# Kernel tuning notes

Measured on AMD Instinct MI355X. Metric: run time of the kernel, lower is better.

The kernel has to match this reference:

```python
import jax, jax.numpy as jnp
import numpy as np

K = 8
B = 3.0
DIM = 32
HID = 32
BATCH = 65536
MIN_BW = 1e-3
MIN_BH = 1e-3
MIN_D = 1e-3


def setup_inputs() -> dict:
    key = jax.random.key(0)
    ks = jax.random.split(key, 8)
    L = DIM - 1
    x = jax.random.normal(ks[0], (BATCH, DIM), jnp.float32)
    init_param = jax.random.uniform(ks[1], (3 * K - 1,), jnp.float32, -0.5, 0.5)
    # stacked per-dim FCNN weights; layer l conditions on x[:, :l+1] -> causal zero-mask
    w1 = jax.random.normal(ks[2], (L, L, HID), jnp.float32) * 0.2
    mask = (jnp.arange(L)[None, :] <= jnp.arange(L)[:, None]).astype(jnp.float32)
    w1 = w1 * mask[:, :, None]
    b1 = jax.random.normal(ks[3], (L, HID), jnp.float32) * 0.1
    w2 = jax.random.normal(ks[4], (L, HID, HID), jnp.float32) * 0.2
    b2 = jax.random.normal(ks[5], (L, HID), jnp.float32) * 0.1
    w3 = jax.random.normal(ks[6], (L, HID, 3 * K - 1), jnp.float32) * 0.2
    b3 = jax.random.normal(ks[7], (L, 3 * K - 1), jnp.float32) * 0.1
    return {"x": x, "init_param": init_param, "w1": w1, "b1": b1,
            "w2": w2, "b2": b2, "w3": w3, "b3": b3}


def _rqs_forward(x, Wu, Hu, Du):
    # x: [dim, batch]; Wu, Hu: [dim, batch, K]; Du: [dim, batch, K-1]
    inside = (x >= -B) & (x <= B)
    xc = jnp.clip(x, -B, B)
    # bin widths
    widths = jax.nn.softmax(Wu, axis=-1)
    widths = MIN_BW + (1.0 - MIN_BW * K) * widths
    cw = jnp.cumsum(widths, axis=-1)
    cw = jnp.concatenate([jnp.zeros(cw.shape[:-1] + (1,), cw.dtype), cw], axis=-1)
    cw = 2.0 * B * cw - B
    cw = cw.at[..., 0].set(-B).at[..., -1].set(B)
    widths = cw[..., 1:] - cw[..., :-1]
    # bin heights
    heights = jax.nn.softmax(Hu, axis=-1)
    heights = MIN_BH + (1.0 - MIN_BH * K) * heights
    ch = jnp.cumsum(heights, axis=-1)
    ch = jnp.concatenate([jnp.zeros(ch.shape[:-1] + (1,), ch.dtype), ch], axis=-1)
    ch = 2.0 * B * ch - B
    ch = ch.at[..., 0].set(-B).at[..., -1].set(B)
    heights = ch[..., 1:] - ch[..., :-1]
    # knot derivatives, edges pinned so softplus(const)+min_d = 1
    const = float(np.log(np.exp(1.0 - MIN_D) - 1.0))
    pad = jnp.full(Du.shape[:-1] + (1,), const, Du.dtype)
    derivs = MIN_D + jax.nn.softplus(jnp.concatenate([pad, Du, pad], axis=-1))  # [.., K+1]
    # bin search (searchsorted on cumwidths, eps bump on last edge)
    cw_s = cw.at[..., -1].add(1e-6)
    idx = jnp.sum((xc[..., None] >= cw_s).astype(jnp.int32), axis=-1) - 1
    idx = jnp.clip(idx, 0, K - 1)
    g = lambda a: jnp.take_along_axis(a, idx[..., None], axis=-1)[..., 0]
    in_cw = g(cw)
    in_w = g(widths)
    in_ch = g(ch)
    in_h = g(heights)
    in_delta = g(heights / widths)
    d0 = g(derivs)
    d1 = g(derivs[..., 1:])
    theta = (xc - in_cw) / in_w
    tt = theta * (1.0 - theta)
    num = in_h * (in_delta * theta ** 2 + d0 * tt)
    den = in_delta + (d0 + d1 - 2.0 * in_delta) * tt
    out = in_ch + num / den
    dnum = in_delta ** 2 * (d1 * theta ** 2 + 2.0 * in_delta * tt + d0 * (1.0 - theta) ** 2)
    ld = jnp.log(dnum) - 2.0 * jnp.log(den)
    out = jnp.where(inside, out, x)  # identity tails
    ld = jnp.where(inside, ld, 0.0)
    return out, ld


def reference(x, init_param, w1, b1, w2, b2, w3, b3):
    # all per-dim conditioners at once (w1 is causally masked in setup)
    h1 = jnp.tanh(jnp.einsum('bd,ldh->lbh', x[:, :DIM - 1], w1) + b1[:, None, :])
    h2 = jnp.tanh(jnp.einsum('lbh,lhg->lbg', h1, w2) + b2[:, None, :])
    out = jnp.einsum('lbh,lho->lbo', h2, w3) + b3[:, None, :]  # [dim-1, batch, 3K-1]
    p0 = jnp.broadcast_to(init_param, (1, x.shape[0], 3 * K - 1))
    params = jnp.concatenate([p0, out], axis=0)  # [dim, batch, 3K-1]
    Wu = 2.0 * B * jax.nn.softmax(params[..., :K], axis=-1)
    Hu = 2.0 * B * jax.nn.softmax(params[..., K:2 * K], axis=-1)
    Du = jax.nn.softplus(params[..., 2 * K:])
    z_t, ld = _rqs_forward(x.T, Wu, Hu, Du)  # [dim, batch]
    return z_t.T, jnp.sum(ld, axis=0)
```

## Files before the change

### kernel.cpp

```cpp
#include <hip/hip_runtime.h>
#include <hip/hip_bf16.h>
#include <cmath>

constexpr int KN   = 8;
constexpr int NPAR = 23;
constexpr int DD   = 32;
constexpr float BND   = 3.0f;
constexpr float MINBW = 1e-3f;
constexpr float MIND  = 1e-3f;

#define TPB   64
#define ROWS  64
#define GDIMS 4
#define WST   40
#define PSTF  28
#define RECB  8192

typedef __attribute__((ext_vector_type(8))) short short8;
typedef __attribute__((ext_vector_type(4))) float float4v;

#define RCP(x) __builtin_amdgcn_rcpf(x)

#if __has_builtin(__builtin_amdgcn_exp2f)
#define EXP2(x) __builtin_amdgcn_exp2f(x)
#else
#define EXP2(x) __expf((x) * 0.6931471805599453f)
#endif
#if __has_builtin(__builtin_amdgcn_logf)
#define LOG2F(x) __builtin_amdgcn_logf(x)
#else
#define LOG2F(x) __log2f(x)
#endif
#define MED3(x, lo, hi) __builtin_amdgcn_fmed3f((x), (lo), (hi))

constexpr float L2E = 1.4426950408889634f;
constexpr float LN2 = 0.6931471805599453f;

__device__ __forceinline__ short f2bf(float f) {
    unsigned u = __float_as_uint(f);
    u += 0x7fffu + ((u >> 16) & 1u);
    return (short)(u >> 16);
}

__device__ __forceinline__ int pkbf(float a, float b) {
    union { __hip_bfloat162 v; int i; } u;
    u.v = __float22bfloat162_rn(make_float2(a, b));
    return u.i;
}

__device__ __forceinline__ float4v tanh4v(float4v c) {
    constexpr float C2L = 2.0f * L2E;
    float4v o;
#pragma unroll
    for (int i = 0; i < 4; ++i) {
        float e = EXP2(c[i] * C2L);
        o[i] = fmaf(-2.f, RCP(e + 1.f), 1.f);
    }
    return o;
}

__device__ __forceinline__ float rqs_apply(float xv, const float* p, float& ldout) {
    constexpr float C1 = 2.0f * BND * MINBW;
    constexpr float FC = 2.0f * BND * (1.0f - MINBW * KN);

    float t0w[KN], t0h[KN];
#pragma unroll
    for (int k = 0; k < KN; ++k) t0w[k] = EXP2(p[k]);
#pragma unroll
    for (int k = 0; k < KN; ++k) t0h[k] = EXP2(p[KN + k]);
    float sw = ((t0w[0] + t0w[1]) + (t0w[2] + t0w[3]))
             + ((t0w[4] + t0w[5]) + (t0w[6] + t0w[7]));
    float sh = ((t0h[0] + t0h[1]) + (t0h[2] + t0h[3]))
             + ((t0h[4] + t0h[5]) + (t0h[6] + t0h[7]));
    float r1   = RCP(sw * sh);
    float invw = (2.0f * BND * L2E) * (r1 * sh);
    float invh = (2.0f * BND * L2E) * (r1 * sw);
    float e2w[KN], e2h[KN];
#pragma unroll
    for (int k = 0; k < KN; ++k) e2w[k] = EXP2(t0w[k] * invw);
#pragma unroll
    for (int k = 0; k < KN; ++k) e2h[k] = EXP2(t0h[k] * invh);
    float s2w = ((e2w[0] + e2w[1]) + (e2w[2] + e2w[3]))
              + ((e2w[4] + e2w[5]) + (e2w[6] + e2w[7]));
    float s2h = ((e2h[0] + e2h[1]) + (e2h[2] + e2h[3]))
              + ((e2h[4] + e2h[5]) + (e2h[6] + e2h[7]));
    float r2   = RCP(s2w * s2h);
    float facw = FC * (r2 * s2h);
    float fach = FC * (r2 * s2w);

    float xc = MED3(xv, -BND, BND);

    float w0 = fmaf(facw, e2w[0], C1);
    float h0 = fmaf(fach, e2h[0], C1);
    float in_cw = -BND, in_w = w0, in_ch = -BND, in_h = h0;
    float dl0 = 0.0f, dl1 = p[2 * KN];
    bool e0 = true, e1 = false;
    float cwk = -BND + w0;
    float chk = -BND + h0;
#pragma unroll
    for (int k = 1; k < KN; ++k) {
        float wk = fmaf(facw, e2w[k], C1);
        float hk = fmaf(fach, e2h[k], C1);
        bool c = (xc >= cwk);
        in_cw = c ? cwk : in_cw;
        in_w  = c ? wk  : in_w;
        in_ch = c ? chk : in_ch;
        in_h  = c ? hk  : in_h;
        dl0   = c ? p[2 * KN + k - 1] : dl0;
        if (k < KN - 1) dl1 = c ? p[2 * KN + k] : dl1;
        if (k == 1)      e0 = !c;
        if (k == KN - 1) e1 = c;
        cwk += wk;
        chk += hk;
    }
    in_w = e1 ? (BND - in_cw) : in_w;
    in_h = e1 ? (BND - in_ch) : in_h;

    float sp0 = LOG2F(2.0f + EXP2(dl0));
    float sp1 = LOG2F(2.0f + EXP2(dl1));
    float d0 = e0 ? 1.0f : fmaf(LN2, sp0, MIND);
    float d1 = e1 ? 1.0f : fmaf(LN2, sp1, MIND);

    float u  = xc - in_cw;
    float v  = in_w - u;
    float s  = in_w, h = in_h;
    float uu = u * u, vv = v * v, uv = u * v;
    float uvs = uv * s;
    float t   = fmaf(v, v, uu);
    float dd  = d0 + d1;
    float DEN = fmaf(h, t, dd * uvs);
    float rD  = RCP(DEN);
    float NUM = fmaf(h, uu, d0 * uvs);
    float z   = fmaf(h * NUM, rD, in_ch);
    float t2  = fmaf(d0, vv, d1 * uu);
    float DN  = fmaf(h + h, uv, t2 * s);
    float h2s = (h * h) * s;
    float larg = ((h2s * DN) * rD) * rD;

    bool inside = (xv >= -BND) && (xv <= BND);
    ldout = inside ? LN2 * LOG2F(larg) : 0.0f;
    return inside ? z : xv;
}

__device__ __forceinline__ short8 xpose_h(float4v cA, float4v cB,
                                          int sl_a, int sl_b, bool qlow) {
    float4v tA = tanh4v(cA);
    float4v tB = tanh4v(cB);
    int a0 = pkbf(tA[0], tA[1]);
    int a1 = pkbf(tA[2], tA[3]);
    int b0 = pkbf(tB[0], tB[1]);
    int b1 = pkbf(tB[2], tB[3]);
    int gA0 = __shfl(a0, sl_a, 64);
    int gA1 = __shfl(a1, sl_a, 64);
    int gA2 = __shfl(a0, sl_b, 64);
    int gA3 = __shfl(a1, sl_b, 64);
    int gB0 = __shfl(b0, sl_a, 64);
    int gB1 = __shfl(b1, sl_a, 64);
    int gB2 = __shfl(b0, sl_b, 64);
    int gB3 = __shfl(b1, sl_b, 64);
    union { int4 i; short8 s; } u;
    u.i = qlow ? make_int4(gA0, gA1, gA2, gA3) : make_int4(gB0, gB1, gB2, gB3);
    return u.s;
}

__device__ __forceinline__ float4v f4v(float4 v) {
    float4v r; r[0] = v.x; r[1] = v.y; r[2] = v.z; r[3] = v.w; return r;
}

struct WFrag {
    short8 w1a, w1b, w2a, w2b, w3a, w3b;
    float4v bA1, bB1, bA2, bB2, bA3, bB3;
};

__device__ __forceinline__ WFrag load_wfrag(const char* __restrict__ wbuf,
                                            int l, int ln, int q) {
    const char* rec = wbuf + (size_t)l * RECB;
    const short* rw = (const short*)rec;
    const float* rb = (const float*)(rec + 7680);
    WFrag f;
    f.w1a = *(const short8*)&rw[ln * WST + q * 8];
    f.w1b = *(const short8*)&rw[(16 + ln) * WST + q * 8];
    f.w2a = *(const short8*)&rw[1280 + ln * WST + q * 8];
    f.w2b = *(const short8*)&rw[1280 + (16 + ln) * WST + q * 8];
    f.w3a = *(const short8*)&rw[2560 + ln * WST + q * 8];
    f.w3b = *(const short8*)&rw[2560 + (16 + ln) * WST + q * 8];
    f.bA1 = f4v(*(const float4*)&rb[4 * q]);
    f.bB1 = f4v(*(const float4*)&rb[16 + 4 * q]);
    f.bA2 = f4v(*(const float4*)&rb[32 + 4 * q]);
    f.bB2 = f4v(*(const float4*)&rb[48 + 4 * q]);
    f.bA3 = f4v(*(const float4*)&rb[64 + 4 * q]);
    f.bB3 = f4v(*(const float4*)&rb[80 + 4 * q]);
    return f;
}

extern "C" __global__ void __launch_bounds__(256)
k_prep(const float* __restrict__ w1, const float* __restrict__ b1,
       const float* __restrict__ w2, const float* __restrict__ b2,
       const float* __restrict__ w3, const float* __restrict__ b3,
       char* __restrict__ wbuf, float* __restrict__ ldo, int B)
{
    const int l = blockIdx.x, tid = threadIdx.x;
    if (l >= 31) {
        const int zb = l - 31;
        const int chunk = B >> 6;
        float4* dst = (float4*)(ldo + (size_t)zb * chunk);
        for (int i = tid; i < (chunk >> 2); i += 256)
            dst[i] = make_float4(0.f, 0.f, 0.f, 0.f);
        return;
    }
    short* r1 = (short*)(wbuf + (size_t)l * RECB);
    short* r2 = r1 + 1280;
    short* r3 = r2 + 1280;
    float* f1 = (float*)(wbuf + (size_t)l * RECB + 7680);
    float* f2 = f1 + 32;
    float* f3 = f2 + 32;
    const float* g1 = w1 + (size_t)l * 992;
    const float* g2 = w2 + (size_t)l * 1024;
    const float* g3 = w3 + (size_t)l * 736;
    for (int i = tid; i < 1280; i += 256) {
        int n = i / WST, k = i - WST * n;
        r1[i] = (k < 31) ? f2bf(g1[k * 32 + n]) : (short)0;
        r2[i] = (k < 32) ? f2bf(g2[k * 32 + n]) : (short)0;
        r3[i] = (n < 23 && k < 32) ? f2bf(g3[k * 23 + n] * L2E) : (short)0;
    }
    if (tid < 32) { f1[tid] = b1[(size_t)l * 32 + tid]; f2[tid] = b2[(size_t)l * 32 + tid]; }
    if (tid < 32) f3[tid] = (tid < 23) ? b3[(size_t)l * 23 + tid] * L2E : 0.0f;
}

extern "C" __global__ void __launch_bounds__(TPB, 2)
k_nsf(const float* __restrict__ x,
      const float* __restrict__ p0,
      const char* __restrict__ wbuf,
      float* __restrict__ zo, float* __restrict__ ldo, int B)
{
    __shared__ __align__(16) float sPf[ROWS * PSTF];

    const int tid  = threadIdx.x;
    const int lane = tid & 63;
    const int q    = lane >> 4;
    const int ln   = lane & 15;
    const int qb   = q & 1;
    const bool qlow = (q < 2);
    const int sl_a = ln + 32 * qb;
    const int sl_b = sl_a + 16;
    const int g    = blockIdx.y;
    const int ly0  = GDIMS * g;
    const long long rowbase = (long long)blockIdx.x * ROWS;
    const long long row = rowbase + tid;

    float xarr[GDIMS];
    {
        float4 xs = *(const float4*)(x + row * DD + ly0);
        xarr[0] = xs.x; xarr[1] = xs.y; xarr[2] = xs.z; xarr[3] = xs.w;
    }

    short8 au[4];
#pragma unroll
    for (int t = 0; t < 4; ++t) {
        const int m0 = 16 * t;
        const float4* xp = (const float4*)(x + (rowbase + m0 + ln) * DD + q * 8);
        float4 uu = xp[0], vv = xp[1];
        union { int4 i; short8 s; } c;
        c.i = make_int4(pkbf(uu.x, uu.y), pkbf(uu.z, uu.w),
                        pkbf(vv.x, vv.y), pkbf(vv.z, vv.w));
        au[t] = c.s;
    }

    float zreg[GDIMS];
    float ldacc = 0.0f;

    WFrag wf = load_wfrag(wbuf, (ly0 == 0) ? 0 : ly0 - 1, ln, q);

#pragma unroll
    for (int j = 0; j < GDIMS; ++j) {
        const int ly = ly0 + j;
        if (ly == 0) {
            float pr[NPAR];
#pragma unroll
            for (int k = 0; k < NPAR; ++k) pr[k] = p0[k] * L2E;
            float ld;
            zreg[0] = rqs_apply(xarr[0], pr, ld);
            ldacc += ld;
            continue;
        }

        float4v cA[4], cB[4];
#pragma unroll
        for (int t = 0; t < 4; ++t) {
            cA[t] = __builtin_amdgcn_mfma_f32_16x16x32_bf16(wf.w1a, au[t], wf.bA1, 0, 0, 0);
            cB[t] = __builtin_amdgcn_mfma_f32_16x16x32_bf16(wf.w1b, au[t], wf.bB1, 0, 0, 0);
        }
        short8 h1f[4];
#pragma unroll
        for (int t = 0; t < 4; ++t)
            h1f[t] = xpose_h(cA[t], cB[t], sl_a, sl_b, qlow);
#pragma unroll
        for (int t = 0; t < 4; ++t) {
            cA[t] = __builtin_amdgcn_mfma_f32_16x16x32_bf16(wf.w2a, h1f[t], wf.bA2, 0, 0, 0);
            cB[t] = __builtin_amdgcn_mfma_f32_16x16x32_bf16(wf.w2b, h1f[t], wf.bB2, 0, 0, 0);
        }
#pragma unroll
        for (int t = 0; t < 4; ++t)
            h1f[t] = xpose_h(cA[t], cB[t], sl_a, sl_b, qlow);
#pragma unroll
        for (int t = 0; t < 4; ++t) {
            cA[t] = __builtin_amdgcn_mfma_f32_16x16x32_bf16(wf.w3a, h1f[t], wf.bA3, 0, 0, 0);
            cB[t] = __builtin_amdgcn_mfma_f32_16x16x32_bf16(wf.w3b, h1f[t], wf.bB3, 0, 0, 0);
        }
#pragma unroll
        for (int t = 0; t < 4; ++t) {
            const int m0 = 16 * t;
            *(float4v*)&sPf[(m0 + ln) * PSTF + 4 * q] = cA[t];
            if (qlow)
                *(float4v*)&sPf[(m0 + ln) * PSTF + 16 + 4 * q] = cB[t];
        }

        WFrag wfn;
        if (j + 1 < GDIMS) wfn = load_wfrag(wbuf, ly, ln, q);

        {
            const float* pp = &sPf[tid * PSTF];
            float pr[24];
#pragma unroll
            for (int u = 0; u < 6; ++u) {
                float4v hv = *(const float4v*)(pp + 4 * u);
                pr[4*u+0] = hv[0];
                pr[4*u+1] = hv[1];
                pr[4*u+2] = hv[2];
                pr[4*u+3] = hv[3];
            }
            float ld;
            zreg[j] = rqs_apply(xarr[j], pr, ld);
            ldacc += ld;
        }
        if (j + 1 < GDIMS) wf = wfn;
    }

    float4 zv = make_float4(zreg[0], zreg[1], zreg[2], zreg[3]);
    *(float4*)(zo + row * DD + ly0) = zv;
    unsafeAtomicAdd(&ldo[row], ldacc);
}

extern "C" void kernel_launch(void* const* d_in, const int* in_sizes, int n_in,
                              void* d_out, int out_size, void* d_ws, size_t ws_size,
                              hipStream_t stream) {
    const float* x  = (const float*)d_in[0];
    const float* p0 = (const float*)d_in[1];
    const float* w1 = (const float*)d_in[2];
    const float* b1 = (const float*)d_in[3];
    const float* w2 = (const float*)d_in[4];
    const float* b2 = (const float*)d_in[5];
    const float* w3 = (const float*)d_in[6];
    const float* b3 = (const float*)d_in[7];

    const int B = in_sizes[0] / DD;
    float* zo  = (float*)d_out;
    float* ldo = zo + (size_t)B * DD;
    char* wbuf = (char*)d_ws;

    hipLaunchKernelGGL(k_prep, dim3(95), dim3(256), 0, stream,
                       w1, b1, w2, b2, w3, b3, wbuf, ldo, B);
    hipLaunchKernelGGL(k_nsf, dim3(B / ROWS, DD / GDIMS), dim3(TPB), 0, stream,
                       x, p0, wbuf, zo, ldo, B);
}
```

Measured before the change: 132.3 us.

## Software-pipeline spline evaluation behind next dim's MFMAs and fold tanh scale

Restructures the per-dimension loop so the rational-quadratic spline for the previous dimension is evaluated after issuing the MFMA conditioner for the current dimension, double-buffering the parameter registers. This aims to overlap matrix-core latency with VALU transcendental work. It also folds the 2*log2(e) tanh scale into the packed w1/w2/b1/b2 weights, removing a multiply per activation. The change raises register pressure and alters bf16 rounding of scaled weights slightly.

```diff
diff --git a/kernel.cpp b/kernel.cpp
--- a/kernel.cpp
+++ b/kernel.cpp
@@ -34,6 +34,7 @@
 #define MED3(x, lo, hi) __builtin_amdgcn_fmed3f((x), (lo), (hi))
 
 constexpr float L2E = 1.4426950408889634f;
+constexpr float C2L = 2.0f * L2E;
 constexpr float LN2 = 0.6931471805599453f;
 
 __device__ __forceinline__ short f2bf(float f) {
@@ -49,11 +50,10 @@
 }
 
 __device__ __forceinline__ float4v tanh4v(float4v c) {
-    constexpr float C2L = 2.0f * L2E;
     float4v o;
 #pragma unroll
     for (int i = 0; i < 4; ++i) {
-        float e = EXP2(c[i] * C2L);
+        float e = EXP2(c[i]);
         o[i] = fmaf(-2.f, RCP(e + 1.f), 1.f);
     }
     return o;
@@ -219,11 +219,11 @@
     const float* g3 = w3 + (size_t)l * 736;
     for (int i = tid; i < 1280; i += 256) {
         int n = i / WST, k = i - WST * n;
-        r1[i] = (k < 31) ? f2bf(g1[k * 32 + n]) : (short)0;
-        r2[i] = (k < 32) ? f2bf(g2[k * 32 + n]) : (short)0;
+        r1[i] = (k < 31) ? f2bf(g1[k * 32 + n] * C2L) : (short)0;
+        r2[i] = (k < 32) ? f2bf(g2[k * 32 + n] * C2L) : (short)0;
         r3[i] = (n < 23 && k < 32) ? f2bf(g3[k * 23 + n] * L2E) : (short)0;
     }
-    if (tid < 32) { f1[tid] = b1[(size_t)l * 32 + tid]; f2[tid] = b2[(size_t)l * 32 + tid]; }
+    if (tid < 32) { f1[tid] = b1[(size_t)l * 32 + tid] * C2L; f2[tid] = b2[(size_t)l * 32 + tid] * C2L; }
     if (tid < 32) f3[tid] = (tid < 23) ? b3[(size_t)l * 23 + tid] * L2E : 0.0f;
 }
 
@@ -268,72 +268,76 @@
 
     float zreg[GDIMS];
     float ldacc = 0.0f;
+    float pr[2][24];
 
     WFrag wf = load_wfrag(wbuf, (ly0 == 0) ? 0 : ly0 - 1, ln, q);
 
 #pragma unroll
     for (int j = 0; j < GDIMS; ++j) {
-        const int ly = ly0 + j;
+        const int ly  = ly0 + j;
+        const int cur = j & 1;
+        WFrag wfn;
         if (ly == 0) {
-            float pr[NPAR];
-#pragma unroll
-            for (int k = 0; k < NPAR; ++k) pr[k] = p0[k] * L2E;
+#pragma unroll
+            for (int k = 0; k < NPAR; ++k) pr[0][k] = p0[k] * L2E;
+        } else {
+            float4v cA[4], cB[4];
+#pragma unroll
+            for (int t = 0; t < 4; ++t) {
+                cA[t] = __builtin_amdgcn_mfma_f32_16x16x32_bf16(wf.w1a, au[t], wf.bA1, 0, 0, 0);
+                cB[t] = __builtin_amdgcn_mfma_f32_16x16x32_bf16(wf.w1b, au[t], wf.bB1, 0, 0, 0);
+            }
+            short8 h1f[4];
+#pragma unroll
+            for (int t = 0; t < 4; ++t)
+                h1f[t] = xpose_h(cA[t], cB[t], sl_a, sl_b, qlow);
+#pragma unroll
+            for (int t = 0; t < 4; ++t) {
+                cA[t] = __builtin_amdgcn_mfma_f32_16x16x32_bf16(wf.w2a, h1f[t], wf.bA2, 0, 0, 0);
+                cB[t] = __builtin_amdgcn_mfma_f32_16x16x32_bf16(wf.w2b, h1f[t], wf.bB2, 0, 0, 0);
+            }
+#pragma unroll
+            for (int t = 0; t < 4; ++t)
+                h1f[t] = xpose_h(cA[t], cB[t], sl_a, sl_b, qlow);
+#pragma unroll
+            for (int t = 0; t < 4; ++t) {
+                cA[t] = __builtin_amdgcn_mfma_f32_16x16x32_bf16(wf.w3a, h1f[t], wf.bA3, 0, 0, 0);
+                cB[t] = __builtin_amdgcn_mfma_f32_16x16x32_bf16(wf.w3b, h1f[t], wf.bB3, 0, 0, 0);
+            }
+#pragma unroll
+            for (int t = 0; t < 4; ++t) {
+                const int m0 = 16 * t;
+                *(float4v*)&sPf[(m0 + ln) * PSTF + 4 * q] = cA[t];
+                if (qlow)
+                    *(float4v*)&sPf[(m0 + ln) * PSTF + 16 + 4 * q] = cB[t];
+            }
+
+            if (j + 1 < GDIMS) wfn = load_wfrag(wbuf, ly, ln, q);
+
+            {
+                const float* pp = &sPf[tid * PSTF];
+#pragma unroll
+                for (int u = 0; u < 6; ++u) {
+                    float4v hv = *(const float4v*)(pp + 4 * u);
+                    pr[cur][4*u+0] = hv[0];
+                    pr[cur][4*u+1] = hv[1];
+                    pr[cur][4*u+2] = hv[2];
+                    pr[cur][4*u+3] = hv[3];
+                }
+            }
+        }
+
+        if (j > 0) {
             float ld;
-            zreg[0] = rqs_apply(xarr[0], pr, ld);
-            ldacc += ld;
-            continue;
-        }
-
-        float4v cA[4], cB[4];
-#pragma unroll
-        for (int t = 0; t < 4; ++t) {
-            cA[t] = __builtin_amdgcn_mfma_f32_16x16x32_bf16(wf.w1a, au[t], wf.bA1, 0, 0, 0);
-            cB[t] = __builtin_amdgcn_mfma_f32_16x16x32_bf16(wf.w1b, au[t], wf.bB1, 0, 0, 0);
-        }
-        short8 h1f[4];
-#pragma unroll
-        for (int t = 0; t < 4; ++t)
-            h1f[t] = xpose_h(cA[t], cB[t], sl_a, sl_b, qlow);
-#pragma unroll
-        for (int t = 0; t < 4; ++t) {
-            cA[t] = __builtin_amdgcn_mfma_f32_16x16x32_bf16(wf.w2a, h1f[t], wf.bA2, 0, 0, 0);
-            cB[t] = __builtin_amdgcn_mfma_f32_16x16x32_bf16(wf.w2b, h1f[t], wf.bB2, 0, 0, 0);
-        }
-#pragma unroll
-        for (int t = 0; t < 4; ++t)
-            h1f[t] = xpose_h(cA[t], cB[t], sl_a, sl_b, qlow);
-#pragma unroll
-        for (int t = 0; t < 4; ++t) {
-            cA[t] = __builtin_amdgcn_mfma_f32_16x16x32_bf16(wf.w3a, h1f[t], wf.bA3, 0, 0, 0);
-            cB[t] = __builtin_amdgcn_mfma_f32_16x16x32_bf16(wf.w3b, h1f[t], wf.bB3, 0, 0, 0);
-        }
-#pragma unroll
-        for (int t = 0; t < 4; ++t) {
-            const int m0 = 16 * t;
-            *(float4v*)&sPf[(m0 + ln) * PSTF + 4 * q] = cA[t];
-            if (qlow)
-                *(float4v*)&sPf[(m0 + ln) * PSTF + 16 + 4 * q] = cB[t];
-        }
-
-        WFrag wfn;
-        if (j + 1 < GDIMS) wfn = load_wfrag(wbuf, ly, ln, q);
-
-        {
-            const float* pp = &sPf[tid * PSTF];
-            float pr[24];
-#pragma unroll
-            for (int u = 0; u < 6; ++u) {
-                float4v hv = *(const float4v*)(pp + 4 * u);
-                pr[4*u+0] = hv[0];
-                pr[4*u+1] = hv[1];
-                pr[4*u+2] = hv[2];
-                pr[4*u+3] = hv[3];
-            }
-            float ld;
-            zreg[j] = rqs_apply(xarr[j], pr, ld);
+            zreg[j-1] = rqs_apply(xarr[j-1], pr[(j-1) & 1], ld);
             ldacc += ld;
         }
-        if (j + 1 < GDIMS) wf = wfn;
+        if (ly != 0 && j + 1 < GDIMS) wf = wfn;
+    }
+    {
+        float ld;
+        zreg[GDIMS-1] = rqs_apply(xarr[GDIMS-1], pr[(GDIMS-1) & 1], ld);
+        ldacc += ld;
     }
 
     float4 zv = make_float4(zreg[0], zreg[1], zreg[2], zreg[3]);
```

Measured after the change: 130.4 us (median of 2 runs). Within noise of the previous version (-1.4%).
